# Kernel optimization log

Hardware: AMD Instinct MI355X
Metric: run time of the kernel (lower is better)

The kernel has to match this reference:

```python
import jax, jax.numpy as jnp
import numpy as np

B, L, V, D, H, C = 2048, 200, 50000, 300, 128, 20


def setup_inputs() -> dict:
    key = jax.random.key(0)
    k = jax.random.split(key, 7)
    x = jax.random.randint(k[0], (B, L), 0, V)
    lengths = jax.random.randint(k[1], (B,), 1, L + 1)  # avoid div-by-zero
    emb_table = jax.random.normal(k[2], (V, D), dtype=jnp.float32)
    W_new = jax.random.normal(k[3], (H, 2 * D), dtype=jnp.float32) * 0.02
    b_new = jax.random.normal(k[4], (H,), dtype=jnp.float32) * 0.02
    W3 = jax.random.normal(k[5], (C, H), dtype=jnp.float32) * 0.02
    b3 = jax.random.normal(k[6], (C,), dtype=jnp.float32) * 0.02
    return {"x": x, "lengths": lengths, "emb_table": emb_table,
            "W_new": W_new, "b_new": b_new, "W3": W3, "b3": b3}


def reference(x, lengths, emb_table, W_new, b_new, W3, b3):
    # [B, L, D] embedding gather
    emb = emb_table[x]
    len_f = lengths.astype(emb.dtype)[:, None]          # [B, 1]
    s = jnp.sum(emb, axis=1)                            # [B, D]
    mx = jnp.max(emb, axis=1)                           # [B, D] (max over padded length, as in original)
    # Original bug preserved: 'mean' feature is sum / lengths^2 (divided twice)
    mean_bug = s / (len_f * len_f)                      # [B, D]
    rep = jnp.concatenate([mean_bug, mx], axis=-1)      # [B, 2D]
    h = jax.nn.relu(rep @ W_new.T + b_new)              # [B, H]
    logits2 = h @ W3.T + b3                             # [B, C]
    return logits2
```

## Files before the change

kernel.cpp:

```cpp
#include <hip/hip_runtime.h>
#include <math.h>

#define B_ 2048
#define L_ 200
#define V_ 50000
#define D_ 300
#define H_ 128
#define C_ 20

__global__ __launch_bounds__(256, 4) void gather_reduce_kernel(
    const int* __restrict__ x,
    const int* __restrict__ lengths,
    const float* __restrict__ emb,
    float* __restrict__ rep)
{
    __shared__ int s_idx[L_];
    __shared__ float4 s_sum[225];
    __shared__ float4 s_max[225];

    const int b = blockIdx.x;
    const int t = threadIdx.x;

    if (t < L_) s_idx[t] = x[b * L_ + t];
    __syncthreads();

    if (t < 225) {
        const int g = t / 75;
        const int p = t - g * 75;
        float4 s4 = make_float4(0.f, 0.f, 0.f, 0.f);
        float4 m4 = make_float4(-INFINITY, -INFINITY, -INFINITY, -INFINITY);
        #pragma unroll 4
        for (int l = g; l < L_; l += 3) {
            const float4 v =
                *(const float4*)(emb + (size_t)s_idx[l] * D_ + (p << 2));
            s4.x += v.x; s4.y += v.y; s4.z += v.z; s4.w += v.w;
            m4.x = fmaxf(m4.x, v.x); m4.y = fmaxf(m4.y, v.y);
            m4.z = fmaxf(m4.z, v.z); m4.w = fmaxf(m4.w, v.w);
        }
        s_sum[t] = s4;
        s_max[t] = m4;
    }
    __syncthreads();

    if (t < 75) {
        const float4 sa = s_sum[t], sb = s_sum[t + 75], sc = s_sum[t + 150];
        const float4 ma = s_max[t], mb = s_max[t + 75], mc = s_max[t + 150];
        const float lf = (float)lengths[b];
        const float inv = 1.0f / (lf * lf);
        float4 S, M;
        S.x = (sa.x + sb.x + sc.x) * inv;
        S.y = (sa.y + sb.y + sc.y) * inv;
        S.z = (sa.z + sb.z + sc.z) * inv;
        S.w = (sa.w + sb.w + sc.w) * inv;
        M.x = fmaxf(fmaxf(ma.x, mb.x), mc.x);
        M.y = fmaxf(fmaxf(ma.y, mb.y), mc.y);
        M.z = fmaxf(fmaxf(ma.z, mb.z), mc.z);
        M.w = fmaxf(fmaxf(ma.w, mb.w), mc.w);
        float4* o = (float4*)(rep + (size_t)b * (2 * D_));
        o[t]      = S;
        o[75 + t] = M;
    }
}

__global__ __launch_bounds__(256, 4) void mlp_kernel(
    const float* __restrict__ rep,
    const float* __restrict__ W_new,
    const float* __restrict__ b_new,
    const float* __restrict__ W3,
    const float* __restrict__ b3,
    float* __restrict__ out)
{
    __shared__ float s_rep[8 * 2 * D_];
    __shared__ float s_h[8][H_ + 4];

    const int t = threadIdx.x;
    const int row0 = blockIdx.x * 8;

    {
        const float4* src = (const float4*)(rep + (size_t)row0 * (2 * D_));
        float4* dst = (float4*)s_rep;
        for (int i = t; i < 1200; i += 256) dst[i] = src[i];
    }
    __syncthreads();

    const int rp = (t >> 6) * 2;
    const int cp = t & 63;
    float a00 = 0.f, a01 = 0.f, a10 = 0.f, a11 = 0.f;

    const float4* w0 = (const float4*)(W_new + (size_t)cp * (2 * D_));
    const float4* w1 = (const float4*)(W_new + (size_t)(cp + 64) * (2 * D_));
    const float4* ra = (const float4*)(s_rep + rp * (2 * D_));
    const float4* rb = (const float4*)(s_rep + (rp + 1) * (2 * D_));

    #pragma unroll 5
    for (int q = 0; q < 150; ++q) {
        const float4 va = ra[q];
        const float4 vb = rb[q];
        const float4 wa = w0[q];
        const float4 wb = w1[q];
        a00 = fmaf(va.x, wa.x, a00); a00 = fmaf(va.y, wa.y, a00);
        a00 = fmaf(va.z, wa.z, a00); a00 = fmaf(va.w, wa.w, a00);
        a01 = fmaf(va.x, wb.x, a01); a01 = fmaf(va.y, wb.y, a01);
        a01 = fmaf(va.z, wb.z, a01); a01 = fmaf(va.w, wb.w, a01);
        a10 = fmaf(vb.x, wa.x, a10); a10 = fmaf(vb.y, wa.y, a10);
        a10 = fmaf(vb.z, wa.z, a10); a10 = fmaf(vb.w, wa.w, a10);
        a11 = fmaf(vb.x, wb.x, a11); a11 = fmaf(vb.y, wb.y, a11);
        a11 = fmaf(vb.z, wb.z, a11); a11 = fmaf(vb.w, wb.w, a11);
    }

    const float bn0 = b_new[cp];
    const float bn1 = b_new[cp + 64];
    s_h[rp    ][cp     ] = fmaxf(a00 + bn0, 0.f);
    s_h[rp    ][cp + 64] = fmaxf(a01 + bn1, 0.f);
    s_h[rp + 1][cp     ] = fmaxf(a10 + bn0, 0.f);
    s_h[rp + 1][cp + 64] = fmaxf(a11 + bn1, 0.f);
    __syncthreads();

    if (t < 8 * C_) {
        const int r = t / C_;
        const int c = t - r * C_;
        const float* hr = s_h[r];
        const float* w3 = W3 + c * H_;
        float acc = b3[c];
        #pragma unroll 8
        for (int k = 0; k < H_; ++k) acc = fmaf(hr[k], w3[k], acc);
        out[(size_t)(row0 + r) * C_ + c] = acc;
    }
}

extern "C" void kernel_launch(void* const* d_in, const int* in_sizes, int n_in,
                              void* d_out, int out_size, void* d_ws, size_t ws_size,
                              hipStream_t stream) {
    const int*   x       = (const int*)  d_in[0];
    const int*   lengths = (const int*)  d_in[1];
    const float* emb     = (const float*)d_in[2];
    const float* W_new   = (const float*)d_in[3];
    const float* b_new   = (const float*)d_in[4];
    const float* W3      = (const float*)d_in[5];
    const float* b3      = (const float*)d_in[6];
    float* out = (float*)d_out;
    float* rep = (float*)d_ws;

    gather_reduce_kernel<<<B_, 256, 0, stream>>>(x, lengths, emb, rep);
    mlp_kernel<<<B_ / 8, 256, 0, stream>>>(rep, W_new, b_new, W3, b3, out);
}
```

Measured before the change: 186.5 us.

## Fuse gather-reduce and MLP into one per-row kernel with batched gather loads

```diff
diff --git a/kernel.cpp b/kernel.cpp
--- a/kernel.cpp
+++ b/kernel.cpp
@@ -8,15 +8,21 @@
 #define H_ 128
 #define C_ 20
 
-__global__ __launch_bounds__(256, 4) void gather_reduce_kernel(
+__global__ __launch_bounds__(256, 4) void fused_dnn_kernel(
     const int* __restrict__ x,
     const int* __restrict__ lengths,
     const float* __restrict__ emb,
-    float* __restrict__ rep)
+    const float* __restrict__ W_new,
+    const float* __restrict__ b_new,
+    const float* __restrict__ W3,
+    const float* __restrict__ b3,
+    float* __restrict__ out)
 {
-    __shared__ int s_idx[L_];
+    __shared__ int    s_idx[L_];
     __shared__ float4 s_sum[225];
     __shared__ float4 s_max[225];
+    __shared__ float4 s_rep4[150];
+    __shared__ float  s_h[H_];
 
     const int b = blockIdx.x;
     const int t = threadIdx.x;
@@ -27,12 +33,36 @@
     if (t < 225) {
         const int g = t / 75;
         const int p = t - g * 75;
+        const int col = p << 2;
         float4 s4 = make_float4(0.f, 0.f, 0.f, 0.f);
         float4 m4 = make_float4(-INFINITY, -INFINITY, -INFINITY, -INFINITY);
-        #pragma unroll 4
-        for (int l = g; l < L_; l += 3) {
+
+        int l = g;
+        for (; l + 9 < L_; l += 12) {
+            const size_t r0 = (size_t)s_idx[l    ] * D_;
+            const size_t r1 = (size_t)s_idx[l + 3] * D_;
+            const size_t r2 = (size_t)s_idx[l + 6] * D_;
+            const size_t r3 = (size_t)s_idx[l + 9] * D_;
+            const float4 v0 = *(const float4*)(emb + r0 + col);
+            const float4 v1 = *(const float4*)(emb + r1 + col);
+            const float4 v2 = *(const float4*)(emb + r2 + col);
+            const float4 v3 = *(const float4*)(emb + r3 + col);
+            s4.x += v0.x; s4.y += v0.y; s4.z += v0.z; s4.w += v0.w;
+            m4.x = fmaxf(m4.x, v0.x); m4.y = fmaxf(m4.y, v0.y);
+            m4.z = fmaxf(m4.z, v0.z); m4.w = fmaxf(m4.w, v0.w);
+            s4.x += v1.x; s4.y += v1.y; s4.z += v1.z; s4.w += v1.w;
+            m4.x = fmaxf(m4.x, v1.x); m4.y = fmaxf(m4.y, v1.y);
+            m4.z = fmaxf(m4.z, v1.z); m4.w = fmaxf(m4.w, v1.w);
+            s4.x += v2.x; s4.y += v2.y; s4.z += v2.z; s4.w += v2.w;
+            m4.x = fmaxf(m4.x, v2.x); m4.y = fmaxf(m4.y, v2.y);
+            m4.z = fmaxf(m4.z, v2.z); m4.w = fmaxf(m4.w, v2.w);
+            s4.x += v3.x; s4.y += v3.y; s4.z += v3.z; s4.w += v3.w;
+            m4.x = fmaxf(m4.x, v3.x); m4.y = fmaxf(m4.y, v3.y);
+            m4.z = fmaxf(m4.z, v3.z); m4.w = fmaxf(m4.w, v3.w);
+        }
+        for (; l < L_; l += 3) {
             const float4 v =
-                *(const float4*)(emb + (size_t)s_idx[l] * D_ + (p << 2));
+                *(const float4*)(emb + (size_t)s_idx[l] * D_ + col);
             s4.x += v.x; s4.y += v.y; s4.z += v.z; s4.w += v.w;
             m4.x = fmaxf(m4.x, v.x); m4.y = fmaxf(m4.y, v.y);
             m4.z = fmaxf(m4.z, v.z); m4.w = fmaxf(m4.w, v.w);
@@ -56,75 +86,47 @@
         M.y = fmaxf(fmaxf(ma.y, mb.y), mc.y);
         M.z = fmaxf(fmaxf(ma.z, mb.z), mc.z);
         M.w = fmaxf(fmaxf(ma.w, mb.w), mc.w);
-        float4* o = (float4*)(rep + (size_t)b * (2 * D_));
-        o[t]      = S;
-        o[75 + t] = M;
-    }
-}
-
-__global__ __launch_bounds__(256, 4) void mlp_kernel(
-    const float* __restrict__ rep,
-    const float* __restrict__ W_new,
-    const float* __restrict__ b_new,
-    const float* __restrict__ W3,
-    const float* __restrict__ b3,
-    float* __restrict__ out)
-{
-    __shared__ float s_rep[8 * 2 * D_];
-    __shared__ float s_h[8][H_ + 4];
-
-    const int t = threadIdx.x;
-    const int row0 = blockIdx.x * 8;
-
-    {
-        const float4* src = (const float4*)(rep + (size_t)row0 * (2 * D_));
-        float4* dst = (float4*)s_rep;
-        for (int i = t; i < 1200; i += 256) dst[i] = src[i];
+        s_rep4[t]      = S;
+        s_rep4[75 + t] = M;
     }
     __syncthreads();
 
-    const int rp = (t >> 6) * 2;
-    const int cp = t & 63;
-    float a00 = 0.f, a01 = 0.f, a10 = 0.f, a11 = 0.f;
+    {
+        const int lane2 = t & 3;
+        const int cbase = t >> 2;
 
-    const float4* w0 = (const float4*)(W_new + (size_t)cp * (2 * D_));
-    const float4* w1 = (const float4*)(W_new + (size_t)(cp + 64) * (2 * D_));
-    const float4* ra = (const float4*)(s_rep + rp * (2 * D_));
-    const float4* rb = (const float4*)(s_rep + (rp + 1) * (2 * D_));
-
-    #pragma unroll 5
-    for (int q = 0; q < 150; ++q) {
-        const float4 va = ra[q];
-        const float4 vb = rb[q];
-        const float4 wa = w0[q];
-        const float4 wb = w1[q];
-        a00 = fmaf(va.x, wa.x, a00); a00 = fmaf(va.y, wa.y, a00);
-        a00 = fmaf(va.z, wa.z, a00); a00 = fmaf(va.w, wa.w, a00);
-        a01 = fmaf(va.x, wb.x, a01); a01 = fmaf(va.y, wb.y, a01);
-        a01 = fmaf(va.z, wb.z, a01); a01 = fmaf(va.w, wb.w, a01);
-        a10 = fmaf(vb.x, wa.x, a10); a10 = fmaf(vb.y, wa.y, a10);
-        a10 = fmaf(vb.z, wa.z, a10); a10 = fmaf(vb.w, wa.w, a10);
-        a11 = fmaf(vb.x, wb.x, a11); a11 = fmaf(vb.y, wb.y, a11);
-        a11 = fmaf(vb.z, wb.z, a11); a11 = fmaf(vb.w, wb.w, a11);
+        #pragma unroll
+        for (int pass = 0; pass < 2; ++pass) {
+            const int c = cbase + (pass << 6);
+            const float4* wrow = (const float4*)(W_new + (size_t)c * (2 * D_));
+            float acc = 0.f;
+            #pragma unroll 4
+            for (int i = 0; i < 38; ++i) {
+                const int q = lane2 + (i << 2);
+                if (q < 150) {
+                    const float4 w = wrow[q];
+                    const float4 r = s_rep4[q];
+                    acc = fmaf(w.x, r.x, acc);
+                    acc = fmaf(w.y, r.y, acc);
+                    acc = fmaf(w.z, r.z, acc);
+                    acc = fmaf(w.w, r.w, acc);
+                }
+            }
+            acc += __shfl_xor(acc, 1);
+            acc += __shfl_xor(acc, 2);
+            if (lane2 == 0) {
+                s_h[c] = fmaxf(acc + b_new[c], 0.f);
+            }
+        }
     }
-
-    const float bn0 = b_new[cp];
-    const float bn1 = b_new[cp + 64];
-    s_h[rp    ][cp     ] = fmaxf(a00 + bn0, 0.f);
-    s_h[rp    ][cp + 64] = fmaxf(a01 + bn1, 0.f);
-    s_h[rp + 1][cp     ] = fmaxf(a10 + bn0, 0.f);
-    s_h[rp + 1][cp + 64] = fmaxf(a11 + bn1, 0.f);
     __syncthreads();
 
-    if (t < 8 * C_) {
-        const int r = t / C_;
-        const int c = t - r * C_;
-        const float* hr = s_h[r];
-        const float* w3 = W3 + c * H_;
-        float acc = b3[c];
-        #pragma unroll 8
-        for (int k = 0; k < H_; ++k) acc = fmaf(hr[k], w3[k], acc);
-        out[(size_t)(row0 + r) * C_ + c] = acc;
+    if (t < C_) {
+        const float* w3 = W3 + t * H_;
+        float acc = b3[t];
+        #pragma unroll 16
+        for (int k = 0; k < H_; ++k) acc = fmaf(s_h[k], w3[k], acc);
+        out[(size_t)b * C_ + t] = acc;
     }
 }
 
@@ -139,8 +141,6 @@
     const float* W3      = (const float*)d_in[5];
     const float* b3      = (const float*)d_in[6];
     float* out = (float*)d_out;
-    float* rep = (float*)d_ws;
 
-    gather_reduce_kernel<<<B_, 256, 0, stream>>>(x, lengths, emb, rep);
-    mlp_kernel<<<B_ / 8, 256, 0, stream>>>(rep, W_new, b_new, W3, b3, out);
+    fused_dnn_kernel<<<B_, 256, 0, stream>>>(x, lengths, emb, W_new, b_new, W3, b3, out);
 }
```

Result: slower. 191.7 us (+2.8%).

## Restructure MLP kernel so each thread reuses weight loads across eight rows

Applied to the files above, without the earlier changes.

```diff
diff --git a/kernel.cpp b/kernel.cpp
--- a/kernel.cpp
+++ b/kernel.cpp
@@ -62,7 +62,7 @@
     }
 }
 
-__global__ __launch_bounds__(256, 4) void mlp_kernel(
+__global__ __launch_bounds__(256) void mlp8_kernel(
     const float* __restrict__ rep,
     const float* __restrict__ W_new,
     const float* __restrict__ b_new,
@@ -70,50 +70,69 @@
     const float* __restrict__ b3,
     float* __restrict__ out)
 {
-    __shared__ float s_rep[8 * 2 * D_];
-    __shared__ float s_h[8][H_ + 4];
+    __shared__ float4 s_rep[8][150];
+    __shared__ float  s_h[8][H_ + 4];
 
     const int t = threadIdx.x;
     const int row0 = blockIdx.x * 8;
 
     {
         const float4* src = (const float4*)(rep + (size_t)row0 * (2 * D_));
-        float4* dst = (float4*)s_rep;
-        for (int i = t; i < 1200; i += 256) dst[i] = src[i];
+        float4* dst = (float4*)&s_rep[0][0];
+        #pragma unroll
+        for (int i = 0; i < 5; ++i) {
+            const int j = t + (i << 8);
+            if (j < 1200) dst[j] = src[j];
+        }
     }
     __syncthreads();
 
-    const int rp = (t >> 6) * 2;
-    const int cp = t & 63;
-    float a00 = 0.f, a01 = 0.f, a10 = 0.f, a11 = 0.f;
+    const int lane2 = t & 3;
+    const int c0 = t >> 2;
+    const int c1 = c0 + 64;
 
-    const float4* w0 = (const float4*)(W_new + (size_t)cp * (2 * D_));
-    const float4* w1 = (const float4*)(W_new + (size_t)(cp + 64) * (2 * D_));
-    const float4* ra = (const float4*)(s_rep + rp * (2 * D_));
-    const float4* rb = (const float4*)(s_rep + (rp + 1) * (2 * D_));
+    float acc0[8] = {0.f, 0.f, 0.f, 0.f, 0.f, 0.f, 0.f, 0.f};
+    float acc1[8] = {0.f, 0.f, 0.f, 0.f, 0.f, 0.f, 0.f, 0.f};
 
-    #pragma unroll 5
-    for (int q = 0; q < 150; ++q) {
-        const float4 va = ra[q];
-        const float4 vb = rb[q];
-        const float4 wa = w0[q];
-        const float4 wb = w1[q];
-        a00 = fmaf(va.x, wa.x, a00); a00 = fmaf(va.y, wa.y, a00);
-        a00 = fmaf(va.z, wa.z, a00); a00 = fmaf(va.w, wa.w, a00);
-        a01 = fmaf(va.x, wb.x, a01); a01 = fmaf(va.y, wb.y, a01);
-        a01 = fmaf(va.z, wb.z, a01); a01 = fmaf(va.w, wb.w, a01);
-        a10 = fmaf(vb.x, wa.x, a10); a10 = fmaf(vb.y, wa.y, a10);
-        a10 = fmaf(vb.z, wa.z, a10); a10 = fmaf(vb.w, wa.w, a10);
-        a11 = fmaf(vb.x, wb.x, a11); a11 = fmaf(vb.y, wb.y, a11);
-        a11 = fmaf(vb.z, wb.z, a11); a11 = fmaf(vb.w, wb.w, a11);
+    const float4* w0row = (const float4*)(W_new + (size_t)c0 * (2 * D_));
+    const float4* w1row = (const float4*)(W_new + (size_t)c1 * (2 * D_));
+
+    #pragma unroll 2
+    for (int i = 0; i < 38; ++i) {
+        const int q = lane2 + (i << 2);
+        if (q < 150) {
+            const float4 w0 = w0row[q];
+            const float4 w1 = w1row[q];
+            #pragma unroll
+            for (int r = 0; r < 8; ++r) {
+                const float4 rq = s_rep[r][q];
+                acc0[r] = fmaf(w0.x, rq.x, acc0[r]);
+                acc0[r] = fmaf(w0.y, rq.y, acc0[r]);
+                acc0[r] = fmaf(w0.z, rq.z, acc0[r]);
+                acc0[r] = fmaf(w0.w, rq.w, acc0[r]);
+                acc1[r] = fmaf(w1.x, rq.x, acc1[r]);
+                acc1[r] = fmaf(w1.y, rq.y, acc1[r]);
+                acc1[r] = fmaf(w1.z, rq.z, acc1[r]);
+                acc1[r] = fmaf(w1.w, rq.w, acc1[r]);
+            }
+        }
     }
 
-    const float bn0 = b_new[cp];
-    const float bn1 = b_new[cp + 64];
-    s_h[rp    ][cp     ] = fmaxf(a00 + bn0, 0.f);
-    s_h[rp    ][cp + 64] = fmaxf(a01 + bn1, 0.f);
-    s_h[rp + 1][cp     ] = fmaxf(a10 + bn0, 0.f);
-    s_h[rp + 1][cp + 64] = fmaxf(a11 + bn1, 0.f);
+    const float bn0 = b_new[c0];
+    const float bn1 = b_new[c1];
+    #pragma unroll
+    for (int r = 0; r < 8; ++r) {
+        float a0 = acc0[r];
+        a0 += __shfl_xor(a0, 1);
+        a0 += __shfl_xor(a0, 2);
+        float a1 = acc1[r];
+        a1 += __shfl_xor(a1, 1);
+        a1 += __shfl_xor(a1, 2);
+        if (lane2 == 0) {
+            s_h[r][c0] = fmaxf(a0 + bn0, 0.f);
+            s_h[r][c1] = fmaxf(a1 + bn1, 0.f);
+        }
+    }
     __syncthreads();
 
     if (t < 8 * C_) {
@@ -142,5 +161,5 @@
     float* rep = (float*)d_ws;
 
     gather_reduce_kernel<<<B_, 256, 0, stream>>>(x, lengths, emb, rep);
-    mlp_kernel<<<B_ / 8, 256, 0, stream>>>(rep, W_new, b_new, W3, b3, out);
+    mlp8_kernel<<<B_ / 8, 256, 0, stream>>>(rep, W_new, b_new, W3, b3, out);
 }
```

After: 180.9 us. -3.0%, faster.
